# Kernel optimization log

Hardware: AMD Instinct MI355X
Metric: run time of the kernel (lower is better)

The kernel has to match this reference:

```python
import jax, jax.numpy as jnp
import numpy as np

MARGIN = 0.3  # init kwarg, mode='norm'


def _pairwise_dist(X):
    # squared euclidean distances, then safe sqrt (matches euc_dist(X.t()).sqrt())
    sq = jnp.sum(X * X, axis=1)                      # [n]
    d2 = sq[:, None] + sq[None, :] - 2.0 * (X @ X.T)  # [n, n]
    d2 = jnp.maximum(d2, 0.0)
    # safe sqrt: avoid inf derivative at 0 (diagonal); forward value identical
    return jnp.where(d2 > 0.0, jnp.sqrt(jnp.where(d2 > 0.0, d2, 1.0)), 0.0)


def setup_inputs() -> dict:
    key = jax.random.key(0)
    kx, ky = jax.random.split(key)
    X = jax.random.normal(kx, (4096, 2048), dtype=jnp.float32)
    Y = jax.random.randint(ky, (4096,), 0, 128, dtype=jnp.int64)
    return {"X": X, "Y": Y}


def reference(X, Y):
    dist = _pairwise_dist(X)                         # [n, n]
    mask = Y[:, None] == Y[None, :]                  # same-identity mask [n, n]
    inf = jnp.array(jnp.inf, dtype=dist.dtype)
    # hardest positive per anchor: max over same-label entries
    dist_ap = jnp.max(jnp.where(mask, dist, -inf), axis=1)  # [n]
    # hardest negative per anchor: min over different-label entries
    dist_an = jnp.min(jnp.where(mask, inf, dist), axis=1)   # [n]
    # mode == 'norm': mean hinge
    return jnp.mean(jnp.maximum(dist_ap - dist_an + MARGIN, 0.0))
```

## Files before the change

kernel.cpp:

```cpp
#include <hip/hip_runtime.h>
#include <hip/hip_bf16.h>
#include <hip/hip_fp8.h>

typedef __attribute__((ext_vector_type(4))) int i32x4;
typedef __attribute__((ext_vector_type(8))) int i32x8;
typedef __attribute__((ext_vector_type(16))) float f32x16;

#define MARGIN 0.3f
#define BIGF 3.0e38f

__device__ __forceinline__ void gl2lds16(const void* g, void* l) {
    __builtin_amdgcn_global_load_lds(
        (const __attribute__((address_space(1))) void*)g,
        (__attribute__((address_space(3))) void*)l,
        16, 0, 0);
}

__global__ __launch_bounds__(256) void convert_norm_kernel(
    const float* __restrict__ X, unsigned char* __restrict__ Xq,
    float* __restrict__ nrm, unsigned* __restrict__ ap,
    unsigned* __restrict__ an, unsigned* __restrict__ cnt, int K) {
    const int wave = threadIdx.x >> 6, lane = threadIdx.x & 63;
    const int row = blockIdx.x * 4 + wave;
    const float* xr = X + (size_t)row * K;
    unsigned char* xqr = Xq + (size_t)row * K;
    float s = 0.0f;
    for (int c = lane * 8; c < K; c += 64 * 8) {
        float4 v0 = *(const float4*)(xr + c);
        float4 v1 = *(const float4*)(xr + c + 4);
        float f[8] = {v0.x, v0.y, v0.z, v0.w, v1.x, v1.y, v1.z, v1.w};
        union { unsigned char b[8]; uint2 u; } p;
#pragma unroll
        for (int i = 0; i < 8; i++) {
            __hip_fp8_e4m3 q(f[i]);
            p.b[i] = q.__x;
            float d = (float)q;
            s += d * d;
        }
        *(uint2*)(xqr + c) = p.u;
    }
    for (int off = 32; off > 0; off >>= 1) s += __shfl_xor(s, off, 64);
    if (lane == 0) {
        nrm[row] = s;
        ap[row] = 0u;
        an[row] = 0x7F800000u;
        if (row == 0) *cnt = 0u;
    }
}

__global__ __launch_bounds__(512, 2) void gemm_reduce_kernel(
    const unsigned char* __restrict__ Xq, const float* __restrict__ nrm,
    const int* __restrict__ Y, unsigned* __restrict__ ap,
    unsigned* __restrict__ an, unsigned* __restrict__ cnt,
    float* __restrict__ out, int N, int K) {
    __shared__ __align__(16) unsigned char sA[2][32768];
    __shared__ __align__(16) unsigned char sB[2][32768];
    __shared__ int sYr[256], sYc[256];
    __shared__ float sNr[256], sNc[256];
    __shared__ float redmax[4][256], redmin[4][256];
    __shared__ float lsum[8];
    __shared__ unsigned s_done;

    const int tid = threadIdx.x;
    const int wave = tid >> 6;
    const int lane = tid & 63;
    const int m = lane & 31;
    const int h = lane >> 5;
    const int wr = wave >> 2;
    const int wc = wave & 3;

    const int NB = N >> 8;
    const int rowBase = (blockIdx.x / NB) << 8;
    const int colBase = (blockIdx.x % NB) << 8;

    if (tid < 256) {
        sYr[tid] = Y[rowBase + tid];
        sNr[tid] = nrm[rowBase + tid];
    } else {
        const int t = tid - 256;
        sYc[t] = Y[colBase + t];
        sNc[t] = nrm[colBase + t];
    }

    f32x16 acc[4][2];
#pragma unroll
    for (int si = 0; si < 4; si++)
#pragma unroll
        for (int sj = 0; sj < 2; sj++)
#pragma unroll
            for (int rr = 0; rr < 16; rr++) acc[si][sj][rr] = 0.0f;

    const int rsub = lane >> 3;
    const int jc = (lane & 7) ^ rsub;
    const unsigned char* gA = Xq + (size_t)(rowBase + wave * 32 + rsub) * K;
    const unsigned char* gB = Xq + (size_t)(colBase + wave * 32 + rsub) * K;
    const size_t g8 = (size_t)8 * K;

    const int e2 = (m & 7) ^ ((m >> 3) & 3);
    const int nit = K >> 7;

#pragma unroll
    for (int g = 0; g < 4; g++) {
        gl2lds16(gA + g * g8 + ((jc ^ g) << 4), &sA[0][wave * 4096 + g * 1024]);
        gl2lds16(gB + g * g8 + ((jc ^ g) << 4), &sB[0][wave * 4096 + g * 1024]);
    }
    __syncthreads();

    int cur = 0;
    for (int it = 0; it < nit; ++it) {
        const bool pf = (it + 1 < nit);
        const size_t go = (size_t)(it + 1) * 128;
        const unsigned char* cA = sA[cur];
        const unsigned char* cB = sB[cur];
        unsigned char* nA = sA[cur ^ 1] + wave * 4096;
        unsigned char* nB = sB[cur ^ 1] + wave * 4096;

#pragma unroll
        for (int s = 0; s < 2; s++) {
            if (pf) {
                if (s == 0) {
#pragma unroll
                    for (int g = 0; g < 4; g++)
                        gl2lds16(gA + go + g * g8 + ((jc ^ g) << 4), nA + g * 1024);
                } else {
#pragma unroll
                    for (int g = 0; g < 4; g++)
                        gl2lds16(gB + go + g * g8 + ((jc ^ g) << 4), nB + g * 1024);
                }
            }
            const int c0 = s * 4 + h * 2;
            i32x8 af[4], bf[2];
#pragma unroll
            for (int si = 0; si < 4; si++) {
                const unsigned char* base = cA + (wr * 128 + si * 32 + m) * 128;
                i32x4 lo = *(const i32x4*)(base + ((c0 ^ e2) << 4));
                i32x4 hi = *(const i32x4*)(base + (((c0 + 1) ^ e2) << 4));
                af[si] = __builtin_shufflevector(lo, hi, 0, 1, 2, 3, 4, 5, 6, 7);
            }
#pragma unroll
            for (int sj = 0; sj < 2; sj++) {
                const unsigned char* base = cB + (wc * 64 + sj * 32 + m) * 128;
                i32x4 lo = *(const i32x4*)(base + ((c0 ^ e2) << 4));
                i32x4 hi = *(const i32x4*)(base + (((c0 + 1) ^ e2) << 4));
                bf[sj] = __builtin_shufflevector(lo, hi, 0, 1, 2, 3, 4, 5, 6, 7);
            }
            __builtin_amdgcn_s_barrier();
            __builtin_amdgcn_s_setprio(1);
#pragma unroll
            for (int si = 0; si < 4; si++)
#pragma unroll
                for (int sj = 0; sj < 2; sj++)
                    acc[si][sj] = __builtin_amdgcn_mfma_scale_f32_32x32x64_f8f6f4(
                        af[si], bf[sj], acc[si][sj], 0 ,
                        0 , 0, 127 ,
                        0, 127 );
            __builtin_amdgcn_s_setprio(0);
            if (s == 0) __builtin_amdgcn_s_barrier();
        }
        __syncthreads();
        cur ^= 1;
    }

#pragma unroll
    for (int si = 0; si < 4; si++)
#pragma unroll
        for (int reg = 0; reg < 16; reg++) {
            const int row128 = si * 32 + (reg & 3) + 8 * (reg >> 2) + 4 * h;
            const int rIdx = wr * 128 + row128;
            const int yr = sYr[rIdx];
            const float nr = sNr[rIdx];
            float dp = -1.0f, dn = BIGF;
#pragma unroll
            for (int sj = 0; sj < 2; sj++) {
                const int cIdx = wc * 64 + sj * 32 + m;
                float d2 = nr + sNc[cIdx] - 2.0f * acc[si][sj][reg];
                float d = sqrtf(fmaxf(d2, 0.0f));
                bool same = (yr == sYc[cIdx]);
                dp = fmaxf(dp, same ? d : -1.0f);
                dn = fminf(dn, same ? BIGF : d);
            }
            for (int off = 1; off < 32; off <<= 1) {
                dp = fmaxf(dp, __shfl_xor(dp, off, 64));
                dn = fminf(dn, __shfl_xor(dn, off, 64));
            }
            if (m == 0) {
                redmax[wc][rIdx] = dp;
                redmin[wc][rIdx] = dn;
            }
        }
    __syncthreads();

    if (tid < 256) {
        float mx = fmaxf(fmaxf(redmax[0][tid], redmax[1][tid]),
                         fmaxf(redmax[2][tid], redmax[3][tid]));
        float mn = fminf(fminf(redmin[0][tid], redmin[1][tid]),
                         fminf(redmin[2][tid], redmin[3][tid]));
        atomicMax(&ap[rowBase + tid], __float_as_uint(fmaxf(mx, 0.0f)));
        atomicMin(&an[rowBase + tid], __float_as_uint(mn));
    }

    __syncthreads();
    if (tid == 0) {
        __threadfence();
        s_done = atomicAdd(cnt, 1u);
    }
    __syncthreads();
    if (s_done == gridDim.x - 1) {
        __threadfence();
        float s = 0.0f;
        for (int i = tid; i < N; i += 512) {
            unsigned ua = __hip_atomic_load(&ap[i], __ATOMIC_RELAXED,
                                            __HIP_MEMORY_SCOPE_AGENT);
            unsigned ub = __hip_atomic_load(&an[i], __ATOMIC_RELAXED,
                                            __HIP_MEMORY_SCOPE_AGENT);
            s += fmaxf(__uint_as_float(ua) - __uint_as_float(ub) + MARGIN, 0.0f);
        }
        for (int off = 32; off > 0; off >>= 1) s += __shfl_xor(s, off, 64);
        if (lane == 0) lsum[wave] = s;
        __syncthreads();
        if (tid == 0) {
            float t = 0.0f;
#pragma unroll
            for (int w = 0; w < 8; w++) t += lsum[w];
            out[0] = t / (float)N;
        }
    }
}

extern "C" void kernel_launch(void* const* d_in, const int* in_sizes, int n_in,
                              void* d_out, int out_size, void* d_ws, size_t ws_size,
                              hipStream_t stream) {
    const float* X = (const float*)d_in[0];
    const int* Y = (const int*)d_in[1];
    float* out = (float*)d_out;
    const int N = in_sizes[1];
    const int K = in_sizes[0] / N;

    char* ws = (char*)d_ws;
    unsigned char* Xq = (unsigned char*)ws;
    float* nrm = (float*)(ws + (size_t)N * K);
    unsigned* ap = (unsigned*)((char*)nrm + (size_t)N * 4);
    unsigned* an = (unsigned*)((char*)ap + (size_t)N * 4);
    unsigned* cnt = (unsigned*)((char*)an + (size_t)N * 4);

    convert_norm_kernel<<<N / 4, 256, 0, stream>>>(X, Xq, nrm, ap, an, cnt, K);
    const int NB = N / 256;
    gemm_reduce_kernel<<<NB * NB, 512, 0, stream>>>(Xq, nrm, Y, ap, an, cnt,
                                                    out, N, K);
}
```

Baseline: 138.5 us.

## Restructure FP8 GEMM main loop into four-phase interleaved prefetch with explicit vmcnt waits

Splits each K iteration of the MX-FP8 MFMA loop into four smaller phases. Each phase issues two global-to-LDS prefetch loads, reads a reduced set of fragments and runs four MFMAs, replacing the two-phase loop that did eight MFMAs per phase. The per-iteration __syncthreads and the one after the initial load are replaced by explicit s_waitcnt vmcnt plus s_barrier. This lowers live fragment registers and spreads memory traffic across compute to hide latency. In exchange it adds more barriers per iteration and relies on manual vmcnt accounting for correctness.

```diff
diff --git a/kernel.cpp b/kernel.cpp
--- a/kernel.cpp
+++ b/kernel.cpp
@@ -8,12 +8,26 @@
 
 #define MARGIN 0.3f
 #define BIGF 3.0e38f
+
+#define VMCNT(n) asm volatile("s_waitcnt vmcnt(" #n ")" ::: "memory")
 
 __device__ __forceinline__ void gl2lds16(const void* g, void* l) {
     __builtin_amdgcn_global_load_lds(
         (const __attribute__((address_space(1))) void*)g,
         (__attribute__((address_space(3))) void*)l,
         16, 0, 0);
+}
+
+__device__ __forceinline__ f32x16 mx_mfma(i32x8 a, i32x8 b, f32x16 c) {
+    return __builtin_amdgcn_mfma_scale_f32_32x32x64_f8f6f4(
+        a, b, c, 0 , 0 ,
+        0, 127 , 0, 127 );
+}
+
+__device__ __forceinline__ i32x8 ldfrag(const unsigned char* base, int c0, int e2) {
+    i32x4 lo = *(const i32x4*)(base + (((c0)     ^ e2) << 4));
+    i32x4 hi = *(const i32x4*)(base + (((c0 + 1) ^ e2) << 4));
+    return __builtin_shufflevector(lo, hi, 0, 1, 2, 3, 4, 5, 6, 7);
 }
 
 __global__ __launch_bounds__(256) void convert_norm_kernel(
@@ -104,60 +118,100 @@
         gl2lds16(gA + g * g8 + ((jc ^ g) << 4), &sA[0][wave * 4096 + g * 1024]);
         gl2lds16(gB + g * g8 + ((jc ^ g) << 4), &sB[0][wave * 4096 + g * 1024]);
     }
-    __syncthreads();
 
     int cur = 0;
     for (int it = 0; it < nit; ++it) {
-        const bool pf = (it + 1 < nit);
-        const size_t go = (size_t)(it + 1) * 128;
         const unsigned char* cA = sA[cur];
         const unsigned char* cB = sB[cur];
         unsigned char* nA = sA[cur ^ 1] + wave * 4096;
         unsigned char* nB = sB[cur ^ 1] + wave * 4096;
-
-#pragma unroll
-        for (int s = 0; s < 2; s++) {
-            if (pf) {
-                if (s == 0) {
-#pragma unroll
-                    for (int g = 0; g < 4; g++)
-                        gl2lds16(gA + go + g * g8 + ((jc ^ g) << 4), nA + g * 1024);
-                } else {
-#pragma unroll
-                    for (int g = 0; g < 4; g++)
-                        gl2lds16(gB + go + g * g8 + ((jc ^ g) << 4), nB + g * 1024);
-                }
-            }
-            const int c0 = s * 4 + h * 2;
-            i32x8 af[4], bf[2];
-#pragma unroll
-            for (int si = 0; si < 4; si++) {
-                const unsigned char* base = cA + (wr * 128 + si * 32 + m) * 128;
-                i32x4 lo = *(const i32x4*)(base + ((c0 ^ e2) << 4));
-                i32x4 hi = *(const i32x4*)(base + (((c0 + 1) ^ e2) << 4));
-                af[si] = __builtin_shufflevector(lo, hi, 0, 1, 2, 3, 4, 5, 6, 7);
-            }
-#pragma unroll
-            for (int sj = 0; sj < 2; sj++) {
-                const unsigned char* base = cB + (wc * 64 + sj * 32 + m) * 128;
-                i32x4 lo = *(const i32x4*)(base + ((c0 ^ e2) << 4));
-                i32x4 hi = *(const i32x4*)(base + (((c0 + 1) ^ e2) << 4));
-                bf[sj] = __builtin_shufflevector(lo, hi, 0, 1, 2, 3, 4, 5, 6, 7);
-            }
-            __builtin_amdgcn_s_barrier();
-            __builtin_amdgcn_s_setprio(1);
-#pragma unroll
-            for (int si = 0; si < 4; si++)
-#pragma unroll
-                for (int sj = 0; sj < 2; sj++)
-                    acc[si][sj] = __builtin_amdgcn_mfma_scale_f32_32x32x64_f8f6f4(
-                        af[si], bf[sj], acc[si][sj], 0 ,
-                        0 , 0, 127 ,
-                        0, 127 );
-            __builtin_amdgcn_s_setprio(0);
-            if (s == 0) __builtin_amdgcn_s_barrier();
-        }
-        __syncthreads();
+        const bool pf = (it + 1 < nit);
+        const size_t go = (size_t)(it + 1) * 128;
+
+        const unsigned char* rA = cA + (wr * 128 + m) * 128;
+        const unsigned char* rB = cB + (wc * 64 + m) * 128;
+
+        i32x8 af0, af1, bf0, bf1;
+
+        if (pf) {
+            gl2lds16(gA + go + 0 * g8 + ((jc ^ 0) << 4), nA + 0 * 1024);
+            gl2lds16(gA + go + 1 * g8 + ((jc ^ 1) << 4), nA + 1 * 1024);
+            VMCNT(2);
+        } else {
+            VMCNT(0);
+        }
+        __builtin_amdgcn_s_barrier();
+        {
+            const int c0 = h * 2;
+            af0 = ldfrag(rA + 0 * 4096, c0, e2);
+            af1 = ldfrag(rA + 1 * 4096, c0, e2);
+            bf0 = ldfrag(rB + 0 * 4096, c0, e2);
+            bf1 = ldfrag(rB + 1 * 4096, c0, e2);
+        }
+        __builtin_amdgcn_s_setprio(1);
+        acc[0][0] = mx_mfma(af0, bf0, acc[0][0]);
+        acc[0][1] = mx_mfma(af0, bf1, acc[0][1]);
+        acc[1][0] = mx_mfma(af1, bf0, acc[1][0]);
+        acc[1][1] = mx_mfma(af1, bf1, acc[1][1]);
+        __builtin_amdgcn_s_setprio(0);
+        __builtin_amdgcn_s_barrier();
+
+        if (pf) {
+            gl2lds16(gA + go + 2 * g8 + ((jc ^ 2) << 4), nA + 2 * 1024);
+            gl2lds16(gA + go + 3 * g8 + ((jc ^ 3) << 4), nA + 3 * 1024);
+        }
+        {
+            const int c0 = h * 2;
+            af0 = ldfrag(rA + 2 * 4096, c0, e2);
+            af1 = ldfrag(rA + 3 * 4096, c0, e2);
+        }
+        __builtin_amdgcn_s_barrier();
+        __builtin_amdgcn_s_setprio(1);
+        acc[2][0] = mx_mfma(af0, bf0, acc[2][0]);
+        acc[2][1] = mx_mfma(af0, bf1, acc[2][1]);
+        acc[3][0] = mx_mfma(af1, bf0, acc[3][0]);
+        acc[3][1] = mx_mfma(af1, bf1, acc[3][1]);
+        __builtin_amdgcn_s_setprio(0);
+        __builtin_amdgcn_s_barrier();
+
+        if (pf) {
+            gl2lds16(gB + go + 0 * g8 + ((jc ^ 0) << 4), nB + 0 * 1024);
+            gl2lds16(gB + go + 1 * g8 + ((jc ^ 1) << 4), nB + 1 * 1024);
+        }
+        {
+            const int c0 = 4 + h * 2;
+            af0 = ldfrag(rA + 0 * 4096, c0, e2);
+            af1 = ldfrag(rA + 1 * 4096, c0, e2);
+            bf0 = ldfrag(rB + 0 * 4096, c0, e2);
+            bf1 = ldfrag(rB + 1 * 4096, c0, e2);
+        }
+        __builtin_amdgcn_s_barrier();
+        __builtin_amdgcn_s_setprio(1);
+        acc[0][0] = mx_mfma(af0, bf0, acc[0][0]);
+        acc[0][1] = mx_mfma(af0, bf1, acc[0][1]);
+        acc[1][0] = mx_mfma(af1, bf0, acc[1][0]);
+        acc[1][1] = mx_mfma(af1, bf1, acc[1][1]);
+        __builtin_amdgcn_s_setprio(0);
+        __builtin_amdgcn_s_barrier();
+
+        if (pf) {
+            gl2lds16(gB + go + 2 * g8 + ((jc ^ 2) << 4), nB + 2 * 1024);
+            gl2lds16(gB + go + 3 * g8 + ((jc ^ 3) << 4), nB + 3 * 1024);
+        }
+        {
+            const int c0 = 4 + h * 2;
+            af0 = ldfrag(rA + 2 * 4096, c0, e2);
+            af1 = ldfrag(rA + 3 * 4096, c0, e2);
+        }
+        __builtin_amdgcn_s_barrier();
+        __builtin_amdgcn_s_setprio(1);
+        acc[2][0] = mx_mfma(af0, bf0, acc[2][0]);
+        acc[2][1] = mx_mfma(af0, bf1, acc[2][1]);
+        acc[3][0] = mx_mfma(af1, bf0, acc[3][0]);
+        acc[3][1] = mx_mfma(af1, bf1, acc[3][1]);
+        __builtin_amdgcn_s_setprio(0);
+        __builtin_amdgcn_s_barrier();
+
         cur ^= 1;
     }
 
```

New measurement: 147.7 us. 1.07x slower.
